# Kernel optimization log

Hardware: AMD Instinct MI355X
Metric: run time of the kernel (lower is better)

The kernel has to match this reference:

```python
import jax, jax.numpy as jnp
import numpy as np

B, S, H, NH = 2, 2048, 1024, 16
DK = H // NH


def setup_inputs() -> dict:
    key = jax.random.key(0)
    ks = jax.random.split(key, 11)
    sc = 1.0 / np.sqrt(H)
    return {
        "q": jax.random.normal(ks[0], (B, S, H), jnp.float32),
        "v": jax.random.normal(ks[1], (B, S, H), jnp.float32),
        "k": jax.random.normal(ks[2], (B, S, H), jnp.float32),
        "Wq": jax.random.normal(ks[3], (H, H), jnp.float32) * sc,
        "bq": jax.random.normal(ks[4], (H,), jnp.float32) * 0.01,
        "Wk": jax.random.normal(ks[5], (H, H), jnp.float32) * sc,
        "bk": jax.random.normal(ks[6], (H,), jnp.float32) * 0.01,
        "Wv": jax.random.normal(ks[7], (H, H), jnp.float32) * sc,
        "bv": jax.random.normal(ks[8], (H,), jnp.float32) * 0.01,
        "Wo": jax.random.normal(ks[9], (H, H), jnp.float32) * sc,
        "bo": jax.random.normal(ks[10], (H,), jnp.float32) * 0.01,
    }


def reference(q, v, k, Wq, bq, Wk, bk, Wv, bv, Wo, bo):
    b, s, h = q.shape
    # projections; torch Linear computes x @ W.T + b
    qh = (q @ Wq.T + bq).reshape(b, s, NH, DK).transpose(0, 2, 1, 3)  # [B,NH,S,DK]
    kh = (k @ Wk.T + bk).reshape(b, s, NH, DK).transpose(0, 2, 1, 3)
    vh = (v @ Wv.T + bv).reshape(b, s, NH, DK).transpose(0, 2, 1, 3)
    scores = jnp.einsum("bhqd,bhkd->bhqk", qh, kh) / jnp.sqrt(
        jnp.asarray(DK, qh.dtype))  # [B,NH,S,S]
    probs = jax.nn.softmax(scores, axis=-1)
    ctx = jnp.einsum("bhqk,bhkd->bhqd", probs, vh)  # [B,NH,S,DK]
    concat = ctx.transpose(0, 2, 1, 3).reshape(b, s, h)
    return concat @ Wo.T + bo
```

## Files before the change

kernel.cpp:

```cpp
#include <hip/hip_runtime.h>
#include <cstddef>
#include <cstdint>

typedef _Float16 f16x8 __attribute__((ext_vector_type(8)));
typedef _Float16 f16x4 __attribute__((ext_vector_type(4)));
typedef __fp16   h16x2 __attribute__((ext_vector_type(2)));
typedef float    f32x4 __attribute__((ext_vector_type(4)));
typedef float    f32x2 __attribute__((ext_vector_type(2)));

constexpr int B_  = 2;
constexpr int S_  = 2048;
constexpr int H_  = 1024;
constexpr int NH_ = 16;
constexpr int DK_ = 64;
constexpr int M_  = B_ * S_;
constexpr int K_  = H_;

constexpr float SOFF = 4.0f;

#define MFMA32(a, b, c) __builtin_amdgcn_mfma_f32_16x16x32_f16((a), (b), (c), 0, 0, 0)

__device__ __forceinline__ void glds16(const void* g, void* l) {
    __builtin_amdgcn_global_load_lds(
        (const __attribute__((address_space(1))) void*)g,
        (__attribute__((address_space(3))) void*)l, 16, 0, 0);
}

struct CvtArgs {
    const float* s[7];
    _Float16*    d[7];
};

__global__ __launch_bounds__(256) void cvt7(CvtArgs a)
{
    const int bid = blockIdx.x;
    int seg, blk;
    if (bid < 6144) { seg = bid >> 11;               blk = bid & 2047; }
    else            { seg = 3 + ((bid - 6144) >> 9); blk = (bid - 6144) & 511; }
    const int i = (blk * 256 + threadIdx.x) * 8;
    const float4 v0 = *reinterpret_cast<const float4*>(a.s[seg] + i);
    const float4 v1 = *reinterpret_cast<const float4*>(a.s[seg] + i + 4);
    f16x8 o;
    o[0] = (_Float16)v0.x; o[1] = (_Float16)v0.y;
    o[2] = (_Float16)v0.z; o[3] = (_Float16)v0.w;
    o[4] = (_Float16)v1.x; o[5] = (_Float16)v1.y;
    o[6] = (_Float16)v1.z; o[7] = (_Float16)v1.w;
    *reinterpret_cast<f16x8*>(a.d[seg] + i) = o;
}

struct QkvArgs {
    const _Float16* A[3];
    const _Float16* W[3];
    const float*    bias[3];
    _Float16* dstQ;
    _Float16* dstK;
    _Float16* dstV;
    float qscale;
};

__global__ __launch_bounds__(256) void gemm_qkv(QkvArgs args)
{
    constexpr int BM = 128, BN = 128, BK = 64;
    __shared__ __align__(16) _Float16 sm[16384];
    _Float16* As = sm;
    _Float16* Ws = sm + 8192;
    auto Tr = reinterpret_cast<_Float16(*)[64]>(sm);

    const int z = blockIdx.z;
    const _Float16* __restrict__ A = args.A[z];
    const _Float16* __restrict__ W = args.W[z];
    const float* __restrict__ bias = args.bias[z];

    const int t = threadIdx.x;
    const int w = t >> 6, lane = t & 63, quad = lane >> 4, l16 = lane & 15;
    const int m0 = blockIdx.y * BM;
    const int n0 = blockIdx.x * BN;
    const int wr = (w & 1) * 64, wc = (w >> 1) * 64;

    const int srow = lane >> 3;
    const int scol = ((lane & 7) ^ srow) * 8;

    const int rx = (l16 & 7) << 4;

    f32x4 acc[4][4];
#pragma unroll
    for (int i = 0; i < 4; ++i)
#pragma unroll
        for (int j = 0; j < 4; ++j) acc[i][j] = (f32x4){0.f, 0.f, 0.f, 0.f};

    for (int k0 = 0; k0 < K_; k0 += BK) {
#pragma unroll
        for (int c = 0; c < 4; ++c) {
            const int r0 = w * 32 + c * 8;
            glds16(&A[(size_t)(m0 + r0 + srow) * K_ + k0 + scol],
                   As + r0 * 64);
            glds16(&W[(size_t)(n0 + r0 + srow) * K_ + k0 + scol],
                   Ws + r0 * 64);
        }
        __syncthreads();

#pragma unroll
        for (int ks = 0; ks < 2; ++ks) {
            const int off = (ks * 64 + quad * 16) ^ rx;
            f16x8 af[4], bf[4];
#pragma unroll
            for (int i = 0; i < 4; ++i)
                af[i] = *reinterpret_cast<const f16x8*>(
                    reinterpret_cast<const char*>(As) +
                    (wr + i * 16 + l16) * 128 + off);
#pragma unroll
            for (int j = 0; j < 4; ++j)
                bf[j] = *reinterpret_cast<const f16x8*>(
                    reinterpret_cast<const char*>(Ws) +
                    (wc + j * 16 + l16) * 128 + off);
#pragma unroll
            for (int i = 0; i < 4; ++i)
#pragma unroll
                for (int j = 0; j < 4; ++j)
                    acc[i][j] = MFMA32(af[i], bf[j], acc[i][j]);
        }
        __syncthreads();
    }

    const float scale = (z == 0) ? args.qscale : 1.0f;
    float bv[4];
#pragma unroll
    for (int j = 0; j < 4; ++j) bv[j] = bias[n0 + wc + j * 16 + l16];

    if (z == 2) {
#pragma unroll
        for (int i = 0; i < 4; ++i) {
            const int sb = m0 + wr + i * 16 + quad * 4;
            const int b = sb >> 11, s = sb & (S_ - 1);
            const int kt = s >> 4;
            const int w4 = kt & 3, tIdx = kt >> 2;
            const int p16 = tIdx >> 1, sub = tIdx & 1;
#pragma unroll
            for (int j = 0; j < 4; ++j) {
                const int d = wc + j * 16 + l16;
                const int h = blockIdx.x * 2 + (d >> 6);
                const int dt = (d & 63) >> 4;
                f16x4 ov;
#pragma unroll
                for (int r = 0; r < 4; ++r) ov[r] = (_Float16)(acc[i][j][r] + bv[j]);
                _Float16* base = args.dstV + ((size_t)b * NH_ + h) * 131072
                    + (size_t)(((w4 * 16 + p16) * 4 + dt) * 512 + lane * 8 + sub * 4);
                *reinterpret_cast<f16x4*>(base) = ov;
            }
        }
        return;
    }

    _Float16* dst = (z == 0) ? args.dstQ : args.dstK;
    const int b = m0 >> 11, s0 = m0 & (S_ - 1);
#pragma unroll
    for (int ch = 0; ch < 2; ++ch) {
        __syncthreads();
        if ((w >> 1) == ch) {
#pragma unroll
            for (int i = 0; i < 4; ++i)
#pragma unroll
                for (int j = 0; j < 4; ++j)
#pragma unroll
                    for (int r = 0; r < 4; ++r)
                        Tr[wr + i * 16 + quad * 4 + r][j * 16 + l16] =
                            (_Float16)((acc[i][j][r] + bv[j]) * scale);
        }
        __syncthreads();
        const int h = blockIdx.x * 2 + ch;
        _Float16* dbase = dst + ((size_t)(b * NH_ + h) * S_ + s0) * DK_;
#pragma unroll
        for (int p = 0; p < 4; ++p) {
            const int c = t + p * 256;
            *reinterpret_cast<f16x8*>(&dbase[c * 8]) =
                *reinterpret_cast<const f16x8*>(&Tr[c >> 3][(c & 7) * 8]);
        }
    }
}

__global__ __launch_bounds__(256) void gemm_out(
    const _Float16* __restrict__ A, const _Float16* __restrict__ W,
    const float* __restrict__ bias, float* __restrict__ out)
{
    constexpr int BM = 64, BN = 128, BK = 32;
    __shared__ _Float16 As[BM][BK];
    __shared__ _Float16 Ws[BN][BK];

    const int t = threadIdx.x;
    const int w = t >> 6, lane = t & 63, quad = lane >> 4, l16 = lane & 15;
    const int m0 = blockIdx.y * BM;
    const int n0 = blockIdx.x * BN;
    const int wc = w * 32;
    const int srow = lane >> 2, scol = (lane & 3) * 8;

    f32x4 acc[4][2];
#pragma unroll
    for (int i = 0; i < 4; ++i)
#pragma unroll
        for (int j = 0; j < 2; ++j) acc[i][j] = (f32x4){0.f, 0.f, 0.f, 0.f};

    for (int k0 = 0; k0 < K_; k0 += BK) {
        glds16(&A[(size_t)(m0 + w * 16 + srow) * K_ + k0 + scol], &As[w * 16][0]);
        glds16(&W[(size_t)(n0 + w * 32 + srow) * K_ + k0 + scol], &Ws[w * 32][0]);
        glds16(&W[(size_t)(n0 + w * 32 + 16 + srow) * K_ + k0 + scol], &Ws[w * 32 + 16][0]);
        __syncthreads();

        f16x8 af[4], bf[2];
#pragma unroll
        for (int i = 0; i < 4; ++i)
            af[i] = *reinterpret_cast<const f16x8*>(&As[i * 16 + l16][quad * 8]);
#pragma unroll
        for (int j = 0; j < 2; ++j)
            bf[j] = *reinterpret_cast<const f16x8*>(&Ws[wc + j * 16 + l16][quad * 8]);
#pragma unroll
        for (int i = 0; i < 4; ++i)
#pragma unroll
            for (int j = 0; j < 2; ++j)
                acc[i][j] = MFMA32(af[i], bf[j], acc[i][j]);
        __syncthreads();
    }

    float bvv[2];
#pragma unroll
    for (int j = 0; j < 2; ++j) bvv[j] = bias[n0 + wc + j * 16 + l16];

#pragma unroll
    for (int i = 0; i < 4; ++i)
#pragma unroll
        for (int j = 0; j < 2; ++j)
#pragma unroll
            for (int r = 0; r < 4; ++r)
                out[(size_t)(m0 + i * 16 + quad * 4 + r) * H_ +
                    n0 + wc + j * 16 + l16] = acc[i][j][r] + bvv[j];
}

__global__ __launch_bounds__(256) void attn_mfma(
    const _Float16* __restrict__ qh, const _Float16* __restrict__ kh,
    const _Float16* __restrict__ vfrag, _Float16* __restrict__ ctx)
{
    __shared__ float Ob[4][64][36];
    __shared__ float Ls[4][64];
    __shared__ float Linv[64];

    const int t = threadIdx.x;
    const int w = t >> 6, lane = t & 63, quad = lane >> 4, l16 = lane & 15;

    const int lin = blockIdx.x;
    const int xcd = lin & 7, slot = lin >> 3;
    const int bh = xcd + 8 * (slot >> 5);
    const int q0 = (slot & 31) * 64;

    const _Float16* qb = qh + (size_t)bh * S_ * DK_;
    const _Float16* kb = kh + (size_t)bh * S_ * DK_;
    const _Float16* vb = vfrag + (size_t)bh * 131072;

    f16x8 qf[4][2];
#pragma unroll
    for (int qt = 0; qt < 4; ++qt)
#pragma unroll
        for (int h2 = 0; h2 < 2; ++h2)
            qf[qt][h2] = *reinterpret_cast<const f16x8*>(
                &qb[(size_t)(q0 + qt * 16 + l16) * DK_ + h2 * 32 + quad * 8]);

    const f32x4 msoff = (f32x4){-SOFF, -SOFF, -SOFF, -SOFF};

    f32x4 o[4][4];
#pragma unroll
    for (int dt = 0; dt < 4; ++dt)
#pragma unroll
        for (int qt = 0; qt < 4; ++qt) o[dt][qt] = (f32x4){0.f, 0.f, 0.f, 0.f};
    f32x2 lp2[4];
#pragma unroll
    for (int qt = 0; qt < 4; ++qt) lp2[qt] = (f32x2){0.f, 0.f};

    const _Float16* kp = kb + (size_t)(w * 16 + l16) * DK_ + quad * 8;
    const _Float16* vp = vb + (size_t)w * 32768 + lane * 8;

    f32x4 scA[4], scB[4];
    {
        const f16x8 kA0 = *reinterpret_cast<const f16x8*>(kp);
        const f16x8 kA1 = *reinterpret_cast<const f16x8*>(kp + 32);
        const f16x8 kB0 = *reinterpret_cast<const f16x8*>(kp + 64 * DK_);
        const f16x8 kB1 = *reinterpret_cast<const f16x8*>(kp + 64 * DK_ + 32);
        kp += 128 * DK_;
#pragma unroll
        for (int qt = 0; qt < 4; ++qt) {
            f32x4 t0 = MFMA32(kA0, qf[qt][0], msoff);
            scA[qt] = MFMA32(kA1, qf[qt][1], t0);
            f32x4 t1 = MFMA32(kB0, qf[qt][0], msoff);
            scB[qt] = MFMA32(kB1, qf[qt][1], t1);
        }
    }

    for (int p = 0; p < 16; ++p) {
        const _Float16* nk = (p < 15) ? kp : (kp - 128 * DK_);
        const f16x8 nA0 = *reinterpret_cast<const f16x8*>(nk);
        const f16x8 nA1 = *reinterpret_cast<const f16x8*>(nk + 32);
        const f16x8 nB0 = *reinterpret_cast<const f16x8*>(nk + 64 * DK_);
        const f16x8 nB1 = *reinterpret_cast<const f16x8*>(nk + 64 * DK_ + 32);
        kp = nk + 128 * DK_;

        f16x8 vf8[4];
#pragma unroll
        for (int dt = 0; dt < 4; ++dt)
            vf8[dt] = *reinterpret_cast<const f16x8*>(vp + dt * 512);
        vp += 2048;

        f16x8 pf8[4];
#pragma unroll
        for (int qt = 0; qt < 4; ++qt) {
            const float a0 = __builtin_amdgcn_exp2f(scA[qt][0]);
            const float a1 = __builtin_amdgcn_exp2f(scA[qt][1]);
            const float a2 = __builtin_amdgcn_exp2f(scA[qt][2]);
            const float a3 = __builtin_amdgcn_exp2f(scA[qt][3]);
            const float b0 = __builtin_amdgcn_exp2f(scB[qt][0]);
            const float b1 = __builtin_amdgcn_exp2f(scB[qt][1]);
            const float b2 = __builtin_amdgcn_exp2f(scB[qt][2]);
            const float b3 = __builtin_amdgcn_exp2f(scB[qt][3]);
            lp2[qt] += ((f32x2){a0, a1} + (f32x2){a2, a3}) +
                       ((f32x2){b0, b1} + (f32x2){b2, b3});
            h16x2* ph = reinterpret_cast<h16x2*>(&pf8[qt]);
            ph[0] = __builtin_amdgcn_cvt_pkrtz(a0, a1);
            ph[1] = __builtin_amdgcn_cvt_pkrtz(a2, a3);
            ph[2] = __builtin_amdgcn_cvt_pkrtz(b0, b1);
            ph[3] = __builtin_amdgcn_cvt_pkrtz(b2, b3);
        }

        __builtin_amdgcn_s_setprio(1);
#pragma unroll
        for (int dt = 0; dt < 4; ++dt)
#pragma unroll
            for (int qt = 0; qt < 4; ++qt)
                o[dt][qt] = MFMA32(vf8[dt], pf8[qt], o[dt][qt]);
#pragma unroll
        for (int qt = 0; qt < 4; ++qt) {
            f32x4 t0 = MFMA32(nA0, qf[qt][0], msoff);
            scA[qt] = MFMA32(nA1, qf[qt][1], t0);
            f32x4 t1 = MFMA32(nB0, qf[qt][0], msoff);
            scB[qt] = MFMA32(nB1, qf[qt][1], t1);
        }
        __builtin_amdgcn_s_setprio(0);
    }

#pragma unroll
    for (int qt = 0; qt < 4; ++qt) {
        float l = lp2[qt][0] + lp2[qt][1];
        l += __shfl_xor(l, 16);
        l += __shfl_xor(l, 32);
        if (quad == 0) Ls[w][qt * 16 + l16] = l;
    }
    __syncthreads();
    if (t < 64)
        Linv[t] = 1.f / (((Ls[0][t] + Ls[1][t]) + (Ls[2][t] + Ls[3][t])));

    const int b = bh >> 4, hh = bh & 15;
    const int dg = t & 3, qq = t >> 2;
#pragma unroll
    for (int ph = 0; ph < 2; ++ph) {
        __syncthreads();
#pragma unroll
        for (int dl = 0; dl < 2; ++dl) {
            const int dt = ph * 2 + dl;
#pragma unroll
            for (int qt = 0; qt < 4; ++qt)
                *reinterpret_cast<f32x4*>(
                    &Ob[w][qt * 16 + l16][dl * 16 + quad * 4]) = o[dt][qt];
        }
        __syncthreads();
        f32x4 s0 = (f32x4){0.f, 0.f, 0.f, 0.f};
        f32x4 s1 = (f32x4){0.f, 0.f, 0.f, 0.f};
#pragma unroll
        for (int ww = 0; ww < 4; ++ww) {
            s0 += *reinterpret_cast<const f32x4*>(&Ob[ww][qq][dg * 8]);
            s1 += *reinterpret_cast<const f32x4*>(&Ob[ww][qq][dg * 8 + 4]);
        }
        const float li = Linv[qq];
        f16x8 ov;
#pragma unroll
        for (int r = 0; r < 4; ++r) {
            ov[r]     = (_Float16)(s0[r] * li);
            ov[4 + r] = (_Float16)(s1[r] * li);
        }
        *reinterpret_cast<f16x8*>(
            &ctx[((size_t)b * S_ + q0 + qq) * H_ + hh * 64 + ph * 32 + dg * 8]) = ov;
    }
}

extern "C" void kernel_launch(void* const* d_in, const int* in_sizes, int n_in,
                              void* d_out, int out_size, void* d_ws,
                              size_t ws_size, hipStream_t stream)
{
    (void)in_sizes; (void)n_in; (void)out_size; (void)ws_size;
    const float* q  = (const float*)d_in[0];
    const float* v  = (const float*)d_in[1];
    const float* k  = (const float*)d_in[2];
    const float* Wq = (const float*)d_in[3];
    const float* bq = (const float*)d_in[4];
    const float* Wk = (const float*)d_in[5];
    const float* bk = (const float*)d_in[6];
    const float* Wv = (const float*)d_in[7];
    const float* bv = (const float*)d_in[8];
    const float* Wo = (const float*)d_in[9];
    const float* bo = (const float*)d_in[10];
    float* out = (float*)d_out;

    constexpr size_t NACT = (size_t)M_ * K_;
    constexpr size_t NW   = (size_t)H_ * H_;
    _Float16* p = (_Float16*)d_ws;
    _Float16* q16  = p;
    _Float16* k16  = p + NACT;
    _Float16* v16  = p + 2 * NACT;
    _Float16* w16q = p + 3 * NACT;
    _Float16* w16k = w16q + NW;
    _Float16* w16v = w16k + NW;
    _Float16* w16o = w16v + NW;
    _Float16* qhd  = w16o + NW;
    _Float16* khd  = qhd + NACT;
    _Float16* vfr  = khd + NACT;
    _Float16* ctx  = q16;

    CvtArgs ca;
    ca.s[0] = q;  ca.d[0] = q16;
    ca.s[1] = v;  ca.d[1] = v16;
    ca.s[2] = k;  ca.d[2] = k16;
    ca.s[3] = Wq; ca.d[3] = w16q;
    ca.s[4] = Wk; ca.d[4] = w16k;
    ca.s[5] = Wv; ca.d[5] = w16v;
    ca.s[6] = Wo; ca.d[6] = w16o;
    cvt7<<<dim3(8192), 256, 0, stream>>>(ca);

    QkvArgs ga;
    ga.A[0] = q16;  ga.W[0] = w16q; ga.bias[0] = bq;
    ga.A[1] = k16;  ga.W[1] = w16k; ga.bias[1] = bk;
    ga.A[2] = v16;  ga.W[2] = w16v; ga.bias[2] = bv;
    ga.dstQ = qhd;  ga.dstK = khd;  ga.dstV = vfr;
    ga.qscale = 0.125f * 1.4426950408889634f;

    gemm_qkv<<<dim3(H_ / 128, M_ / 128, 3), 256, 0, stream>>>(ga);

    attn_mfma<<<dim3(S_ / 64 * B_ * NH_), 256, 0, stream>>>(qhd, khd, vfr, ctx);

    gemm_out<<<dim3(H_ / 128, M_ / 64), 256, 0, stream>>>(ctx, w16o, bo, out);
}
```

Measured before the change: 228.5 us.

## Split attention block across 8 waves with query halves per wave group

The attention kernel now launches 512 threads per block. Each group of four waves handles half of the 64 query rows (32 rows) while still splitting keys four ways, which halves per-wave registers and accumulators. The intent is more waves resident and better latency hiding for the exp/MFMA loop. The cost is that each K and V fragment is now loaded by two waves, doubling K/V load traffic per block, and the final reduction is reworked to match the new layout.

After: 302.6 us. +32.4%, slower.

```diff
diff --git a/kernel.cpp b/kernel.cpp
--- a/kernel.cpp
+++ b/kernel.cpp
@@ -234,16 +234,17 @@
                     n0 + wc + j * 16 + l16] = acc[i][j][r] + bvv[j];
 }
 
-__global__ __launch_bounds__(256) void attn_mfma(
+__global__ __launch_bounds__(512, 4) void attn_mfma(
     const _Float16* __restrict__ qh, const _Float16* __restrict__ kh,
     const _Float16* __restrict__ vfrag, _Float16* __restrict__ ctx)
 {
-    __shared__ float Ob[4][64][36];
-    __shared__ float Ls[4][64];
+    __shared__ float Ob[8][32][36];
+    __shared__ float Ls[8][32];
     __shared__ float Linv[64];
 
     const int t = threadIdx.x;
     const int w = t >> 6, lane = t & 63, quad = lane >> 4, l16 = lane & 15;
+    const int kg = w & 3, qhf = w >> 2;
 
     const int lin = blockIdx.x;
     const int xcd = lin & 7, slot = lin >> 3;
@@ -254,29 +255,30 @@
     const _Float16* kb = kh + (size_t)bh * S_ * DK_;
     const _Float16* vb = vfrag + (size_t)bh * 131072;
 
-    f16x8 qf[4][2];
-#pragma unroll
-    for (int qt = 0; qt < 4; ++qt)
+    f16x8 qf[2][2];
+#pragma unroll
+    for (int qt = 0; qt < 2; ++qt)
 #pragma unroll
         for (int h2 = 0; h2 < 2; ++h2)
             qf[qt][h2] = *reinterpret_cast<const f16x8*>(
-                &qb[(size_t)(q0 + qt * 16 + l16) * DK_ + h2 * 32 + quad * 8]);
+                &qb[(size_t)(q0 + qhf * 32 + qt * 16 + l16) * DK_ +
+                    h2 * 32 + quad * 8]);
 
     const f32x4 msoff = (f32x4){-SOFF, -SOFF, -SOFF, -SOFF};
 
-    f32x4 o[4][4];
+    f32x4 o[4][2];
 #pragma unroll
     for (int dt = 0; dt < 4; ++dt)
 #pragma unroll
-        for (int qt = 0; qt < 4; ++qt) o[dt][qt] = (f32x4){0.f, 0.f, 0.f, 0.f};
-    f32x2 lp2[4];
-#pragma unroll
-    for (int qt = 0; qt < 4; ++qt) lp2[qt] = (f32x2){0.f, 0.f};
-
-    const _Float16* kp = kb + (size_t)(w * 16 + l16) * DK_ + quad * 8;
-    const _Float16* vp = vb + (size_t)w * 32768 + lane * 8;
-
-    f32x4 scA[4], scB[4];
+        for (int qt = 0; qt < 2; ++qt) o[dt][qt] = (f32x4){0.f, 0.f, 0.f, 0.f};
+    f32x2 lp2[2];
+#pragma unroll
+    for (int qt = 0; qt < 2; ++qt) lp2[qt] = (f32x2){0.f, 0.f};
+
+    const _Float16* kp = kb + (size_t)(kg * 16 + l16) * DK_ + quad * 8;
+    const _Float16* vp = vb + (size_t)kg * 32768 + lane * 8;
+
+    f32x4 scA[2], scB[2];
     {
         const f16x8 kA0 = *reinterpret_cast<const f16x8*>(kp);
         const f16x8 kA1 = *reinterpret_cast<const f16x8*>(kp + 32);
@@ -284,7 +286,7 @@
         const f16x8 kB1 = *reinterpret_cast<const f16x8*>(kp + 64 * DK_ + 32);
         kp += 128 * DK_;
 #pragma unroll
-        for (int qt = 0; qt < 4; ++qt) {
+        for (int qt = 0; qt < 2; ++qt) {
             f32x4 t0 = MFMA32(kA0, qf[qt][0], msoff);
             scA[qt] = MFMA32(kA1, qf[qt][1], t0);
             f32x4 t1 = MFMA32(kB0, qf[qt][0], msoff);
@@ -306,9 +308,9 @@
             vf8[dt] = *reinterpret_cast<const f16x8*>(vp + dt * 512);
         vp += 2048;
 
-        f16x8 pf8[4];
-#pragma unroll
-        for (int qt = 0; qt < 4; ++qt) {
+        f16x8 pf8[2];
+#pragma unroll
+        for (int qt = 0; qt < 2; ++qt) {
             const float a0 = __builtin_amdgcn_exp2f(scA[qt][0]);
             const float a1 = __builtin_amdgcn_exp2f(scA[qt][1]);
             const float a2 = __builtin_amdgcn_exp2f(scA[qt][2]);
@@ -330,10 +332,10 @@
 #pragma unroll
         for (int dt = 0; dt < 4; ++dt)
 #pragma unroll
-            for (int qt = 0; qt < 4; ++qt)
+            for (int qt = 0; qt < 2; ++qt)
                 o[dt][qt] = MFMA32(vf8[dt], pf8[qt], o[dt][qt]);
 #pragma unroll
-        for (int qt = 0; qt < 4; ++qt) {
+        for (int qt = 0; qt < 2; ++qt) {
             f32x4 t0 = MFMA32(nA0, qf[qt][0], msoff);
             scA[qt] = MFMA32(nA1, qf[qt][1], t0);
             f32x4 t1 = MFMA32(nB0, qf[qt][0], msoff);
@@ -343,18 +345,21 @@
     }
 
 #pragma unroll
-    for (int qt = 0; qt < 4; ++qt) {
+    for (int qt = 0; qt < 2; ++qt) {
         float l = lp2[qt][0] + lp2[qt][1];
         l += __shfl_xor(l, 16);
         l += __shfl_xor(l, 32);
         if (quad == 0) Ls[w][qt * 16 + l16] = l;
     }
     __syncthreads();
-    if (t < 64)
-        Linv[t] = 1.f / (((Ls[0][t] + Ls[1][t]) + (Ls[2][t] + Ls[3][t])));
+    if (t < 64) {
+        const int wb = (t >> 5) * 4, r = t & 31;
+        Linv[t] = 1.f / (((Ls[wb + 0][r] + Ls[wb + 1][r]) +
+                          (Ls[wb + 2][r] + Ls[wb + 3][r])));
+    }
 
     const int b = bh >> 4, hh = bh & 15;
-    const int dg = t & 3, qq = t >> 2;
+    const int dg8 = t & 7, qq = t >> 3;
 #pragma unroll
     for (int ph = 0; ph < 2; ++ph) {
         __syncthreads();
@@ -362,27 +367,22 @@
         for (int dl = 0; dl < 2; ++dl) {
             const int dt = ph * 2 + dl;
 #pragma unroll
-            for (int qt = 0; qt < 4; ++qt)
+            for (int qt = 0; qt < 2; ++qt)
                 *reinterpret_cast<f32x4*>(
                     &Ob[w][qt * 16 + l16][dl * 16 + quad * 4]) = o[dt][qt];
         }
         __syncthreads();
-        f32x4 s0 = (f32x4){0.f, 0.f, 0.f, 0.f};
-        f32x4 s1 = (f32x4){0.f, 0.f, 0.f, 0.f};
-#pragma unroll
-        for (int ww = 0; ww < 4; ++ww) {
-            s0 += *reinterpret_cast<const f32x4*>(&Ob[ww][qq][dg * 8]);
-            s1 += *reinterpret_cast<const f32x4*>(&Ob[ww][qq][dg * 8 + 4]);
-        }
+        f32x4 s = (f32x4){0.f, 0.f, 0.f, 0.f};
+        const int wb = (qq >> 5) * 4, r = qq & 31;
+#pragma unroll
+        for (int i = 0; i < 4; ++i)
+            s += *reinterpret_cast<const f32x4*>(&Ob[wb + i][r][dg8 * 4]);
         const float li = Linv[qq];
-        f16x8 ov;
-#pragma unroll
-        for (int r = 0; r < 4; ++r) {
-            ov[r]     = (_Float16)(s0[r] * li);
-            ov[4 + r] = (_Float16)(s1[r] * li);
-        }
-        *reinterpret_cast<f16x8*>(
-            &ctx[((size_t)b * S_ + q0 + qq) * H_ + hh * 64 + ph * 32 + dg * 8]) = ov;
+        f16x4 ov;
+#pragma unroll
+        for (int k = 0; k < 4; ++k) ov[k] = (_Float16)(s[k] * li);
+        *reinterpret_cast<f16x4*>(
+            &ctx[((size_t)b * S_ + q0 + qq) * H_ + hh * 64 + ph * 32 + dg8 * 4]) = ov;
     }
 }
 
@@ -438,7 +438,7 @@
 
     gemm_qkv<<<dim3(H_ / 128, M_ / 128, 3), 256, 0, stream>>>(ga);
 
-    attn_mfma<<<dim3(S_ / 64 * B_ * NH_), 256, 0, stream>>>(qhd, khd, vfr, ctx);
+    attn_mfma<<<dim3(S_ / 64 * B_ * NH_), 512, 0, stream>>>(qhd, khd, vfr, ctx);
 
     gemm_out<<<dim3(H_ / 128, M_ / 64), 256, 0, stream>>>(ctx, w16o, bo, out);
 }
```
